# Optimization experiments

Hardware: AMD Instinct MI355X
Metric: run time of the kernel (lower is better)

Reference implementation:

```python
import jax, jax.numpy as jnp
import numpy as np

H = 16        # num_attention_heads
D = 1024      # hidden_size
HD = D // H   # attention_head_size = 64

def setup_inputs() -> dict:
    key = jax.random.key(0)
    ks = jax.random.split(key, 5)
    scale = 0.02
    return {
        "hidden_states": jax.random.normal(ks[0], (4, 2048, D), dtype=jnp.float32),
        "attention_mask": jnp.zeros((4, 2048), dtype=jnp.float32),
        "Wq": jax.random.normal(ks[1], (D, D), dtype=jnp.float32) * scale,
        "bq": jnp.zeros((D,), dtype=jnp.float32),
        "Wk": jax.random.normal(ks[2], (D, D), dtype=jnp.float32) * scale,
        "bk": jnp.zeros((D,), dtype=jnp.float32),
        "Wv": jax.random.normal(ks[3], (D, D), dtype=jnp.float32) * scale,
        "bv": jnp.zeros((D,), dtype=jnp.float32),
    }

def _heads(x, B, S):
    # [B,S,D] -> [B,H,S,HD]
    return x.reshape(B, S, H, HD).transpose(0, 2, 1, 3)

def reference(hidden_states, attention_mask, Wq, bq, Wk, bk, Wv, bv):
    B, S, _ = hidden_states.shape
    q = _heads(hidden_states @ Wq + bq, B, S)
    k = _heads(hidden_states @ Wk + bk, B, S)
    v = _heads(hidden_states @ Wv + bv, B, S)
    # scores: [B,H,S,S]
    scores = jnp.einsum('bhqd,bhkd->bhqk', q, k) / jnp.sqrt(jnp.float32(HD))
    scores = scores + attention_mask[:, None, None, :]  # additive mask
    probs = jax.nn.softmax(scores, axis=-1)
    # dropout is identity in eval mode
    ctx = jnp.einsum('bhqk,bhkd->bhqd', probs, v)
    return ctx.transpose(0, 2, 1, 3).reshape(B, S, H * HD)
```

## Files before the change

### kernel.cpp

```cpp
#include <hip/hip_runtime.h>


typedef __bf16 bf16_t;
typedef __bf16 bf16x2 __attribute__((ext_vector_type(2)));
typedef __bf16 bf16x4 __attribute__((ext_vector_type(4)));
typedef __bf16 bf16x8 __attribute__((ext_vector_type(8)));
typedef float floatx16 __attribute__((ext_vector_type(16)));
typedef float floatx4 __attribute__((ext_vector_type(4)));

__device__ __forceinline__ void glds16(const void* g, void* l) {
  __builtin_amdgcn_global_load_lds(
      (const __attribute__((address_space(1))) void*)g,
      (__attribute__((address_space(3))) void*)l, 16, 0, 0);
}

__device__ __forceinline__ float exp2_fast(float x) {
  return __builtin_amdgcn_exp2f(x);
}

__device__ __forceinline__ unsigned pk2(float a, float b) {
  union { bf16x2 v; unsigned u; } cv;
  cv.v[0] = (bf16_t)a; cv.v[1] = (bf16_t)b;
  return cv.u;
}

__global__ __launch_bounds__(256) void k_cvt_x(const float* __restrict__ X,
                                               bf16_t* __restrict__ Xb) {
  int i = (blockIdx.x * 256 + threadIdx.x) * 4;
  float4 v = *(const float4*)(X + i);
  bf16x4 o;
  o[0] = (bf16_t)v.x; o[1] = (bf16_t)v.y; o[2] = (bf16_t)v.z; o[3] = (bf16_t)v.w;
  *(bf16x4*)(Xb + i) = o;
}

__global__ __launch_bounds__(256) void k_tw(const float* __restrict__ Wq,
                                            const float* __restrict__ Wk,
                                            const float* __restrict__ Wv,
                                            bf16_t* __restrict__ Wt) {
  int z = blockIdx.z;
  const float* W = (z == 0) ? Wq : ((z == 1) ? Wk : Wv);
  bf16_t* dst = Wt + (size_t)z * 1048576;
  __shared__ float t[32][33];
  int tx = threadIdx.x & 31, ty = threadIdx.x >> 5;
  int bx = blockIdx.x, by = blockIdx.y;
#pragma unroll
  for (int r = 0; r < 4; r++) {
    int k = by * 32 + ty + r * 8;
    t[ty + r * 8][tx] = W[k * 1024 + bx * 32 + tx];
  }
  __syncthreads();
#pragma unroll
  for (int r = 0; r < 4; r++) {
    int n = bx * 32 + ty + r * 8;
    dst[(size_t)n * 1024 + by * 32 + tx] = (bf16_t)t[tx][ty + r * 8];
  }
}

__global__ __launch_bounds__(256) void k_qkv(
    const bf16_t* __restrict__ Xb, const bf16_t* __restrict__ Wt,
    const float* __restrict__ bq, const float* __restrict__ bk,
    const float* __restrict__ bv, bf16_t* __restrict__ Qb,
    bf16_t* __restrict__ Kb, bf16_t* __restrict__ Vt) {
  __shared__ bf16_t tA[128 * 64];
  __shared__ bf16_t tB[128 * 64];
  int tid = threadIdx.x, wv = tid >> 6, lane = tid & 63;
  int quad = lane >> 4, l16 = lane & 15;
  int wm = wv >> 1, wn = wv & 1;

  int id = blockIdx.x;
  int x = id & 7, w = id >> 3;
  int bn = w >> 3, pm = w & 7;
  int bm = x * 8 + pm;
  size_t m0 = (size_t)bm * 128, n0 = (size_t)bn * 128;
  int wsel = bn >> 3;

  floatx4 acc[4][4];
#pragma unroll
  for (int a = 0; a < 4; a++)
#pragma unroll
    for (int b = 0; b < 4; b++)
#pragma unroll
      for (int r = 0; r < 4; r++) acc[a][b][r] = 0.f;

  const bf16_t* Ab = Xb + m0 * 1024;
  const bf16_t* Bb = Wt + n0 * 1024;
  const bf16_t* fA = (wsel == 2) ? tB : tA;
  const bf16_t* fB = (wsel == 2) ? tA : tB;

  for (int k0 = 0; k0 < 1024; k0 += 64) {
    __syncthreads();
#pragma unroll
    for (int i = 0; i < 4; i++) {
      int j = wv * 4 + i;
      int row = j * 8 + (lane >> 3);
      int dblk = (lane & 7) ^ (row & 7);
      glds16(Ab + (size_t)row * 1024 + k0 + dblk * 8, tA + j * 512);
      glds16(Bb + (size_t)row * 1024 + k0 + dblk * 8, tB + j * 512);
    }
    __syncthreads();
#pragma unroll
    for (int s = 0; s < 2; s++) {
      bf16x8 av[4], bw[4];
#pragma unroll
      for (int rt = 0; rt < 4; rt++) {
        int rowa = wm * 64 + rt * 16 + l16;
        av[rt] = *(const bf16x8*)(fA + rowa * 64 + (((4 * s + quad) ^ (rowa & 7)) * 8));
        int rowb = wn * 64 + rt * 16 + l16;
        bw[rt] = *(const bf16x8*)(fB + rowb * 64 + (((4 * s + quad) ^ (rowb & 7)) * 8));
      }
#pragma unroll
      for (int rt = 0; rt < 4; rt++)
#pragma unroll
        for (int ct = 0; ct < 4; ct++)
          acc[rt][ct] = __builtin_amdgcn_mfma_f32_16x16x32_bf16(av[rt], bw[ct],
                                                               acc[rt][ct], 0, 0, 0);
    }
  }

  if (wsel == 2) {
    int bb = (int)(m0 >> 11);
#pragma unroll
    for (int rt = 0; rt < 4; rt++) {
#pragma unroll
      for (int r = 0; r < 4; r++) {
        int nl = wm * 64 + rt * 16 + quad * 4 + r;
        int n1 = ((int)n0 + nl) & 1023;
        int hh = n1 >> 6, dd = n1 & 63;
        float bi = bv[n1];
        size_t base = (size_t)(bb * 16 + hh) * 131072 + (size_t)dd * 2048;
#pragma unroll
        for (int ct = 0; ct < 4; ct++) {
          int m = (int)m0 + wn * 64 + ct * 16 + l16;
          Vt[base + (m & 2047)] = (bf16_t)(acc[rt][ct][r] + bi);
        }
      }
    }
  } else {
    const float* bias = (wsel == 0) ? bq : bk;
#pragma unroll
    for (int ct = 0; ct < 4; ct++) {
      int n = (int)n0 + wn * 64 + ct * 16 + l16;
      int n1 = n & 1023;
      int hh = n1 >> 6, dd = n1 & 63;
      float bi = bias[n1];
#pragma unroll
      for (int rt = 0; rt < 4; rt++) {
#pragma unroll
        for (int r = 0; r < 4; r++) {
          int m = (int)m0 + wm * 64 + rt * 16 + quad * 4 + r;
          int bb = m >> 11, ss = m & 2047;
          size_t bh = (size_t)(bb * 16 + hh);
          float v = acc[rt][ct][r] + bi;
          if (wsel == 0) {
            Qb[bh * 131072 + (size_t)ss * 64 + dd] = (bf16_t)(v * 0.18033688011117f);
          } else {
            Kb[bh * 131072 + (size_t)ss * 64 + dd] = (bf16_t)v;
          }
        }
      }
    }
  }
}

__global__ __launch_bounds__(256, 3) void k_attn(const bf16_t* __restrict__ Qb,
                                                 const bf16_t* __restrict__ Kb,
                                                 const bf16_t* __restrict__ VtG,
                                                 const float* __restrict__ mask,
                                                 float* __restrict__ out) {
  __shared__ float smem[10240];
  bf16_t* lds = (bf16_t*)smem;
  float* mlds = smem + 8192;

  int tid = threadIdx.x, wq = tid >> 6, lane = tid & 63;
  int q5 = lane & 31, h5 = lane >> 5;

  int id = blockIdx.x;
  int x = id & 7, w = id >> 3;
  int bh = x * 8 + (w >> 4), qt = w & 15;
  int b = bh >> 4, hh = bh & 15;

  const bf16_t* Qp = Qb + (size_t)bh * 131072;
  const bf16_t* Kp = Kb + (size_t)bh * 131072;
  const bf16_t* Vp = VtG + (size_t)bh * 131072;
  const float* mp = mask + b * 2048;

#pragma unroll
  for (int j = 0; j < 2; j++) {
    float4 mv = *(const float4*)(mp + tid * 8 + j * 4);
    float4 sv;
    sv.x = mv.x * 1.4426950408890f - 12.0f;
    sv.y = mv.y * 1.4426950408890f - 12.0f;
    sv.z = mv.z * 1.4426950408890f - 12.0f;
    sv.w = mv.w * 1.4426950408890f - 12.0f;
    *(float4*)(mlds + tid * 8 + j * 4) = sv;
  }

  int q0 = qt * 128 + wq * 32;
  bf16x8 qf[4];
#pragma unroll
  for (int s = 0; s < 4; s++)
    qf[s] = *(const bf16x8*)(Qp + (size_t)(q0 + q5) * 64 + s * 16 + h5 * 8);

  int off[2][4];
#pragma unroll
  for (int j = 0; j < 2; j++)
#pragma unroll
    for (int s = 0; s < 4; s++)
      off[j][s] = (j * 32 + q5) * 64 + (((2 * s + h5) ^ (q5 & 7)) * 8);

  int r0 = wq * 16 + (lane >> 3);
  int slot = (lane & 7) ^ ((lane >> 3) & 7);
  const bf16_t* kg0 = Kp + (size_t)r0 * 64 + slot * 8;
  const bf16_t* kg1 = kg0 + 512;
  const bf16_t* vg0 = Vp + (size_t)r0 * 2048 + slot * 8;
  const bf16_t* vg1 = vg0 + 16384;
  int c0 = wq * 2;

  floatx16 ov[2];
#pragma unroll
  for (int t2 = 0; t2 < 2; t2++)
#pragma unroll
    for (int r = 0; r < 16; r++) ov[t2][r] = 0.f;
  float p0 = 0.f, p1 = 0.f, p2 = 0.f, p3 = 0.f;

  {
    bf16_t* bK = lds;
    bf16_t* bV = lds + 4096;
    glds16(kg0, bK + c0 * 512); glds16(kg1, bK + c0 * 512 + 512);
    glds16(vg0, bV + c0 * 512); glds16(vg1, bV + c0 * 512 + 512);
    kg0 += 4096; kg1 += 4096; vg0 += 64; vg1 += 64;
  }

  for (int it = 0; it < 32; ++it) {
    int kk0 = it * 64, cur = it & 1;
    __syncthreads();
    if (it + 1 < 32) {
      bf16_t* bK = lds + (cur ^ 1) * 8192;
      bf16_t* bV = bK + 4096;
      glds16(kg0, bK + c0 * 512); glds16(kg1, bK + c0 * 512 + 512);
      glds16(vg0, bV + c0 * 512); glds16(vg1, bV + c0 * 512 + 512);
      kg0 += 4096; kg1 += 4096; vg0 += 64; vg1 += 64;
    }
    const bf16_t* bK = lds + cur * 8192;
    const bf16_t* bV = bK + 4096;

    floatx16 st[2];
#pragma unroll
    for (int tt = 0; tt < 2; tt++) {
      floatx16 a;
#pragma unroll
      for (int r = 0; r < 16; r++) a[r] = 0.f;
#pragma unroll
      for (int s = 0; s < 4; s++) {
        bf16x8 kf = *(const bf16x8*)(bK + off[tt][s]);
        a = __builtin_amdgcn_mfma_f32_32x32x16_bf16(kf, qf[s], a, 0, 0, 0);
      }
      st[tt] = a;
    }

#pragma unroll
    for (int tt = 0; tt < 2; tt++) {
#pragma unroll
      for (int g = 0; g < 4; g++) {
        float4 mv = *(const float4*)(mlds + kk0 + tt * 32 + g * 8 + h5 * 4);
        float e0 = exp2_fast(st[tt][g * 4 + 0] + mv.x);
        float e1 = exp2_fast(st[tt][g * 4 + 1] + mv.y);
        float e2 = exp2_fast(st[tt][g * 4 + 2] + mv.z);
        float e3 = exp2_fast(st[tt][g * 4 + 3] + mv.w);
        st[tt][g * 4 + 0] = e0; st[tt][g * 4 + 1] = e1;
        st[tt][g * 4 + 2] = e2; st[tt][g * 4 + 3] = e3;
        p0 += e0; p1 += e1; p2 += e2; p3 += e3;
      }
    }

#pragma unroll
    for (int s = 0; s < 4; s++) {
      int t = s >> 1, base = (s & 1) * 8;
      unsigned A  = pk2(st[t][base + 0], st[t][base + 1]);
      unsigned B2 = pk2(st[t][base + 2], st[t][base + 3]);
      unsigned C  = pk2(st[t][base + 4], st[t][base + 5]);
      unsigned D  = pk2(st[t][base + 6], st[t][base + 7]);
      unsigned s1 = h5 ? A : C, s2 = h5 ? B2 : D;
      unsigned r1 = (unsigned)__shfl_xor((int)s1, 32);
      unsigned r2 = (unsigned)__shfl_xor((int)s2, 32);
      union { uint4 u; bf16x8 v; } pf;
      pf.u.x = h5 ? r1 : A;  pf.u.y = h5 ? r2 : B2;
      pf.u.z = h5 ? C  : r1; pf.u.w = h5 ? D  : r2;
#pragma unroll
      for (int t2 = 0; t2 < 2; t2++) {
        bf16x8 vf = *(const bf16x8*)(bV + off[t2][s]);
        ov[t2] = __builtin_amdgcn_mfma_f32_32x32x16_bf16(vf, pf.v, ov[t2], 0, 0, 0);
      }
    }
  }

  float ls = (p0 + p1) + (p2 + p3);
  ls += __shfl_xor(ls, 32);
  float rl = 1.f / ls;

  __syncthreads();
#pragma unroll
  for (int t2 = 0; t2 < 2; t2++)
#pragma unroll
    for (int r = 0; r < 16; r++) {
      int d = t2 * 32 + (r & 3) + 8 * (r >> 2) + 4 * h5;
      smem[(wq * 32 + q5) * 68 + d] = ov[t2][r] * rl;
    }
  __syncthreads();
  int qbase = b * 2048 + qt * 128;
#pragma unroll
  for (int i = 0; i < 8; i++) {
    int slot2 = i * 256 + tid;
    int q = slot2 >> 4, c = slot2 & 15;
    float4 v = *(const float4*)(smem + q * 68 + c * 4);
    *(float4*)(out + (size_t)(qbase + q) * 1024 + hh * 64 + c * 4) = v;
  }
}

extern "C" void kernel_launch(void* const* d_in, const int* in_sizes, int n_in,
                              void* d_out, int out_size, void* d_ws, size_t ws_size,
                              hipStream_t stream) {
  const float* X    = (const float*)d_in[0];
  const float* mask = (const float*)d_in[1];
  const float* Wq   = (const float*)d_in[2];
  const float* bq   = (const float*)d_in[3];
  const float* Wk   = (const float*)d_in[4];
  const float* bk   = (const float*)d_in[5];
  const float* Wv   = (const float*)d_in[6];
  const float* bv   = (const float*)d_in[7];
  float* out = (float*)d_out;

  char* ws = (char*)d_ws;
  bf16_t* Xb = (bf16_t*)ws;
  bf16_t* Wt = (bf16_t*)(ws + 16777216);
  bf16_t* Qb = (bf16_t*)(ws + 23068672);
  bf16_t* Kb = (bf16_t*)(ws + 39845888);
  bf16_t* Vt = (bf16_t*)(ws + 56623104);

  k_cvt_x<<<8192, 256, 0, stream>>>(X, Xb);
  k_tw<<<dim3(32, 32, 3), 256, 0, stream>>>(Wq, Wk, Wv, Wt);
  k_qkv<<<1536, 256, 0, stream>>>(Xb, Wt, bq, bk, bv, Qb, Kb, Vt);
  k_attn<<<1024, 256, 0, stream>>>(Qb, Kb, Vt, mask, out);
}
```

Before: 253.1 us.

## Double attention block to 8 waves sharing each K/V tile

The attention kernel now launches 512 blocks of 512 threads, each covering 256 queries with 8 waves, so every K/V tile loaded into LDS feeds twice as many waves and each thread issues half as many global-to-LDS loads. The exp2 computation is also interleaved with the bf16 packing per sub-step, which should shorten register live ranges. The output epilogue is split into two halves that reuse the same LDS staging area. In exchange, barriers now synchronise 8 waves instead of 4, and the launch bounds change from 3 to 4 waves per EU, which may pressure registers.

```diff
diff --git a/kernel.cpp b/kernel.cpp
--- a/kernel.cpp
+++ b/kernel.cpp
@@ -162,12 +162,12 @@
   }
 }
 
-__global__ __launch_bounds__(256, 3) void k_attn(const bf16_t* __restrict__ Qb,
+__global__ __launch_bounds__(512, 4) void k_attn(const bf16_t* __restrict__ Qb,
                                                  const bf16_t* __restrict__ Kb,
                                                  const bf16_t* __restrict__ VtG,
                                                  const float* __restrict__ mask,
                                                  float* __restrict__ out) {
-  __shared__ float smem[10240];
+  __shared__ float smem[10752];
   bf16_t* lds = (bf16_t*)smem;
   float* mlds = smem + 8192;
 
@@ -176,7 +176,7 @@
 
   int id = blockIdx.x;
   int x = id & 7, w = id >> 3;
-  int bh = x * 8 + (w >> 4), qt = w & 15;
+  int bh = x * 8 + (w >> 3), qt8 = w & 7;
   int b = bh >> 4, hh = bh & 15;
 
   const bf16_t* Qp = Qb + (size_t)bh * 131072;
@@ -184,18 +184,17 @@
   const bf16_t* Vp = VtG + (size_t)bh * 131072;
   const float* mp = mask + b * 2048;
 
-#pragma unroll
-  for (int j = 0; j < 2; j++) {
-    float4 mv = *(const float4*)(mp + tid * 8 + j * 4);
+  {
+    float4 mv = *(const float4*)(mp + tid * 4);
     float4 sv;
     sv.x = mv.x * 1.4426950408890f - 12.0f;
     sv.y = mv.y * 1.4426950408890f - 12.0f;
     sv.z = mv.z * 1.4426950408890f - 12.0f;
     sv.w = mv.w * 1.4426950408890f - 12.0f;
-    *(float4*)(mlds + tid * 8 + j * 4) = sv;
-  }
-
-  int q0 = qt * 128 + wq * 32;
+    *(float4*)(mlds + tid * 4) = sv;
+  }
+
+  int q0 = qt8 * 256 + wq * 32;
   bf16x8 qf[4];
 #pragma unroll
   for (int s = 0; s < 4; s++)
@@ -208,13 +207,11 @@
     for (int s = 0; s < 4; s++)
       off[j][s] = (j * 32 + q5) * 64 + (((2 * s + h5) ^ (q5 & 7)) * 8);
 
-  int r0 = wq * 16 + (lane >> 3);
+  int r0 = wq * 8 + (lane >> 3);
   int slot = (lane & 7) ^ ((lane >> 3) & 7);
-  const bf16_t* kg0 = Kp + (size_t)r0 * 64 + slot * 8;
-  const bf16_t* kg1 = kg0 + 512;
-  const bf16_t* vg0 = Vp + (size_t)r0 * 2048 + slot * 8;
-  const bf16_t* vg1 = vg0 + 16384;
-  int c0 = wq * 2;
+  const bf16_t* kg = Kp + (size_t)r0 * 64 + slot * 8;
+  const bf16_t* vg = Vp + (size_t)r0 * 2048 + slot * 8;
+  int c512 = wq * 512;
 
   floatx16 ov[2];
 #pragma unroll
@@ -223,23 +220,18 @@
     for (int r = 0; r < 16; r++) ov[t2][r] = 0.f;
   float p0 = 0.f, p1 = 0.f, p2 = 0.f, p3 = 0.f;
 
-  {
-    bf16_t* bK = lds;
-    bf16_t* bV = lds + 4096;
-    glds16(kg0, bK + c0 * 512); glds16(kg1, bK + c0 * 512 + 512);
-    glds16(vg0, bV + c0 * 512); glds16(vg1, bV + c0 * 512 + 512);
-    kg0 += 4096; kg1 += 4096; vg0 += 64; vg1 += 64;
-  }
+  glds16(kg, lds + c512);
+  glds16(vg, lds + 4096 + c512);
+  kg += 4096; vg += 64;
 
   for (int it = 0; it < 32; ++it) {
     int kk0 = it * 64, cur = it & 1;
     __syncthreads();
     if (it + 1 < 32) {
-      bf16_t* bK = lds + (cur ^ 1) * 8192;
-      bf16_t* bV = bK + 4096;
-      glds16(kg0, bK + c0 * 512); glds16(kg1, bK + c0 * 512 + 512);
-      glds16(vg0, bV + c0 * 512); glds16(vg1, bV + c0 * 512 + 512);
-      kg0 += 4096; kg1 += 4096; vg0 += 64; vg1 += 64;
+      bf16_t* bKn = lds + (cur ^ 1) * 8192;
+      glds16(kg, bKn + c512);
+      glds16(vg, bKn + 4096 + c512);
+      kg += 4096; vg += 64;
     }
     const bf16_t* bK = lds + cur * 8192;
     const bf16_t* bV = bK + 4096;
@@ -259,27 +251,24 @@
     }
 
 #pragma unroll
-    for (int tt = 0; tt < 2; tt++) {
-#pragma unroll
-      for (int g = 0; g < 4; g++) {
-        float4 mv = *(const float4*)(mlds + kk0 + tt * 32 + g * 8 + h5 * 4);
-        float e0 = exp2_fast(st[tt][g * 4 + 0] + mv.x);
-        float e1 = exp2_fast(st[tt][g * 4 + 1] + mv.y);
-        float e2 = exp2_fast(st[tt][g * 4 + 2] + mv.z);
-        float e3 = exp2_fast(st[tt][g * 4 + 3] + mv.w);
-        st[tt][g * 4 + 0] = e0; st[tt][g * 4 + 1] = e1;
-        st[tt][g * 4 + 2] = e2; st[tt][g * 4 + 3] = e3;
-        p0 += e0; p1 += e1; p2 += e2; p3 += e3;
-      }
-    }
-
-#pragma unroll
     for (int s = 0; s < 4; s++) {
       int t = s >> 1, base = (s & 1) * 8;
-      unsigned A  = pk2(st[t][base + 0], st[t][base + 1]);
-      unsigned B2 = pk2(st[t][base + 2], st[t][base + 3]);
-      unsigned C  = pk2(st[t][base + 4], st[t][base + 5]);
-      unsigned D  = pk2(st[t][base + 6], st[t][base + 7]);
+      int g0 = (s & 1) * 2;
+      float4 m0v = *(const float4*)(mlds + kk0 + t * 32 + g0 * 8 + h5 * 4);
+      float4 m1v = *(const float4*)(mlds + kk0 + t * 32 + (g0 + 1) * 8 + h5 * 4);
+      float e0 = exp2_fast(st[t][base + 0] + m0v.x);
+      float e1 = exp2_fast(st[t][base + 1] + m0v.y);
+      float e2 = exp2_fast(st[t][base + 2] + m0v.z);
+      float e3 = exp2_fast(st[t][base + 3] + m0v.w);
+      float e4 = exp2_fast(st[t][base + 4] + m1v.x);
+      float e5 = exp2_fast(st[t][base + 5] + m1v.y);
+      float e6 = exp2_fast(st[t][base + 6] + m1v.z);
+      float e7 = exp2_fast(st[t][base + 7] + m1v.w);
+      p0 += e0 + e4; p1 += e1 + e5; p2 += e2 + e6; p3 += e3 + e7;
+      unsigned A  = pk2(e0, e1);
+      unsigned B2 = pk2(e2, e3);
+      unsigned C  = pk2(e4, e5);
+      unsigned D  = pk2(e6, e7);
       unsigned s1 = h5 ? A : C, s2 = h5 ? B2 : D;
       unsigned r1 = (unsigned)__shfl_xor((int)s1, 32);
       unsigned r2 = (unsigned)__shfl_xor((int)s2, 32);
@@ -298,22 +287,29 @@
   ls += __shfl_xor(ls, 32);
   float rl = 1.f / ls;
 
-  __syncthreads();
-#pragma unroll
-  for (int t2 = 0; t2 < 2; t2++)
-#pragma unroll
-    for (int r = 0; r < 16; r++) {
-      int d = t2 * 32 + (r & 3) + 8 * (r >> 2) + 4 * h5;
-      smem[(wq * 32 + q5) * 68 + d] = ov[t2][r] * rl;
-    }
-  __syncthreads();
-  int qbase = b * 2048 + qt * 128;
-#pragma unroll
-  for (int i = 0; i < 8; i++) {
-    int slot2 = i * 256 + tid;
-    int q = slot2 >> 4, c = slot2 & 15;
-    float4 v = *(const float4*)(smem + q * 68 + c * 4);
-    *(float4*)(out + (size_t)(qbase + q) * 1024 + hh * 64 + c * 4) = v;
+  int qbase0 = b * 2048 + qt8 * 256;
+#pragma unroll
+  for (int half = 0; half < 2; half++) {
+    __syncthreads();
+    if ((wq >> 2) == half) {
+      int qloc = (wq & 3) * 32 + q5;
+#pragma unroll
+      for (int t2 = 0; t2 < 2; t2++)
+#pragma unroll
+        for (int r = 0; r < 16; r++) {
+          int d = t2 * 32 + (r & 3) + 8 * (r >> 2) + 4 * h5;
+          smem[qloc * 68 + d] = ov[t2][r] * rl;
+        }
+    }
+    __syncthreads();
+    int qbase = qbase0 + half * 128;
+#pragma unroll
+    for (int i = 0; i < 4; i++) {
+      int slot2 = i * 512 + tid;
+      int q = slot2 >> 4, c = slot2 & 15;
+      float4 v = *(const float4*)(smem + q * 68 + c * 4);
+      *(float4*)(out + (size_t)(qbase + q) * 1024 + hh * 64 + c * 4) = v;
+    }
   }
 }
 
@@ -340,5 +336,5 @@
   k_cvt_x<<<8192, 256, 0, stream>>>(X, Xb);
   k_tw<<<dim3(32, 32, 3), 256, 0, stream>>>(Wq, Wk, Wv, Wt);
   k_qkv<<<1536, 256, 0, stream>>>(Xb, Wt, bq, bk, bv, Qb, Kb, Vt);
-  k_attn<<<1024, 256, 0, stream>>>(Qb, Kb, Vt, mask, out);
-}
+  k_attn<<<512, 512, 0, stream>>>(Qb, Kb, Vt, mask, out);
+}
```

After: 246.2 us. 1.03x faster.

## Double query rows per attention wave, fold mask into MFMA, merge prep kernels

Applied to the files above, without the earlier changes.

Each attention wave now handles 64 query rows instead of 32, so every K/V tile loaded into LDS feeds twice as many MFMAs and the grid halves to 512 blocks. The additive mask is applied through an extra MFMA with a one-hot Q fragment instead of per-element VALU adds, and the epilogue writes output in two halves through shared memory. The X conversion and weight transpose kernels are merged into one launch. The cost is higher register pressure (occupancy hint lowered from 3 to 2), fewer blocks in flight, and the mask value being rounded to bf16.

```diff
diff --git a/kernel.cpp b/kernel.cpp
--- a/kernel.cpp
+++ b/kernel.cpp
@@ -24,35 +24,38 @@
   return cv.u;
 }
 
-__global__ __launch_bounds__(256) void k_cvt_x(const float* __restrict__ X,
-                                               bf16_t* __restrict__ Xb) {
-  int i = (blockIdx.x * 256 + threadIdx.x) * 4;
-  float4 v = *(const float4*)(X + i);
-  bf16x4 o;
-  o[0] = (bf16_t)v.x; o[1] = (bf16_t)v.y; o[2] = (bf16_t)v.z; o[3] = (bf16_t)v.w;
-  *(bf16x4*)(Xb + i) = o;
-}
-
-__global__ __launch_bounds__(256) void k_tw(const float* __restrict__ Wq,
-                                            const float* __restrict__ Wk,
-                                            const float* __restrict__ Wv,
-                                            bf16_t* __restrict__ Wt) {
-  int z = blockIdx.z;
-  const float* W = (z == 0) ? Wq : ((z == 1) ? Wk : Wv);
-  bf16_t* dst = Wt + (size_t)z * 1048576;
-  __shared__ float t[32][33];
-  int tx = threadIdx.x & 31, ty = threadIdx.x >> 5;
-  int bx = blockIdx.x, by = blockIdx.y;
-#pragma unroll
-  for (int r = 0; r < 4; r++) {
-    int k = by * 32 + ty + r * 8;
-    t[ty + r * 8][tx] = W[k * 1024 + bx * 32 + tx];
-  }
-  __syncthreads();
-#pragma unroll
-  for (int r = 0; r < 4; r++) {
-    int n = bx * 32 + ty + r * 8;
-    dst[(size_t)n * 1024 + by * 32 + tx] = (bf16_t)t[tx][ty + r * 8];
+__global__ __launch_bounds__(256) void k_prep(const float* __restrict__ X,
+                                              bf16_t* __restrict__ Xb,
+                                              const float* __restrict__ Wq,
+                                              const float* __restrict__ Wk,
+                                              const float* __restrict__ Wv,
+                                              bf16_t* __restrict__ Wt) {
+  int bid = blockIdx.x;
+  if (bid < 8192) {
+    int i = (bid * 256 + threadIdx.x) * 4;
+    float4 v = *(const float4*)(X + i);
+    bf16x4 o;
+    o[0] = (bf16_t)v.x; o[1] = (bf16_t)v.y; o[2] = (bf16_t)v.z; o[3] = (bf16_t)v.w;
+    *(bf16x4*)(Xb + i) = o;
+  } else {
+    int t = bid - 8192;
+    int z = t >> 10, r2 = t & 1023;
+    int bx = r2 & 31, by = r2 >> 5;
+    const float* W = (z == 0) ? Wq : ((z == 1) ? Wk : Wv);
+    bf16_t* dst = Wt + (size_t)z * 1048576;
+    __shared__ float tt[32][33];
+    int tx = threadIdx.x & 31, ty = threadIdx.x >> 5;
+#pragma unroll
+    for (int r = 0; r < 4; r++) {
+      int k = by * 32 + ty + r * 8;
+      tt[ty + r * 8][tx] = W[k * 1024 + bx * 32 + tx];
+    }
+    __syncthreads();
+#pragma unroll
+    for (int r = 0; r < 4; r++) {
+      int n = bx * 32 + ty + r * 8;
+      dst[(size_t)n * 1024 + by * 32 + tx] = (bf16_t)tt[tx][ty + r * 8];
+    }
   }
 }
 
@@ -162,7 +165,7 @@
   }
 }
 
-__global__ __launch_bounds__(256, 3) void k_attn(const bf16_t* __restrict__ Qb,
+__global__ __launch_bounds__(256, 2) void k_attn(const bf16_t* __restrict__ Qb,
                                                  const bf16_t* __restrict__ Kb,
                                                  const bf16_t* __restrict__ VtG,
                                                  const float* __restrict__ mask,
@@ -176,7 +179,7 @@
 
   int id = blockIdx.x;
   int x = id & 7, w = id >> 3;
-  int bh = x * 8 + (w >> 4), qt = w & 15;
+  int bh = x * 8 + (w >> 3), qt = w & 7;
   int b = bh >> 4, hh = bh & 15;
 
   const bf16_t* Qp = Qb + (size_t)bh * 131072;
@@ -195,11 +198,17 @@
     *(float4*)(mlds + tid * 8 + j * 4) = sv;
   }
 
-  int q0 = qt * 128 + wq * 32;
-  bf16x8 qf[4];
-#pragma unroll
-  for (int s = 0; s < 4; s++)
-    qf[s] = *(const bf16x8*)(Qp + (size_t)(q0 + q5) * 64 + s * 16 + h5 * 8);
+  int q0 = qt * 256 + wq * 64;
+  bf16x8 qf0[4], qf1[4];
+#pragma unroll
+  for (int s = 0; s < 4; s++) {
+    qf0[s] = *(const bf16x8*)(Qp + (size_t)(q0 + q5) * 64 + s * 16 + h5 * 8);
+    qf1[s] = *(const bf16x8*)(Qp + (size_t)(q0 + 32 + q5) * 64 + s * 16 + h5 * 8);
+  }
+
+  union { uint4 u; bf16x8 v; } qfe;
+  qfe.u.x = h5 ? 0u : 0x00003f80u;
+  qfe.u.y = 0u; qfe.u.z = 0u; qfe.u.w = 0u;
 
   int off[2][4];
 #pragma unroll
@@ -216,12 +225,13 @@
   const bf16_t* vg1 = vg0 + 16384;
   int c0 = wq * 2;
 
-  floatx16 ov[2];
-#pragma unroll
-  for (int t2 = 0; t2 < 2; t2++)
+  floatx16 ov[4];
+#pragma unroll
+  for (int t2 = 0; t2 < 4; t2++)
 #pragma unroll
     for (int r = 0; r < 16; r++) ov[t2][r] = 0.f;
-  float p0 = 0.f, p1 = 0.f, p2 = 0.f, p3 = 0.f;
+  float pa0 = 0.f, pa1 = 0.f, pa2 = 0.f, pa3 = 0.f;
+  float pb0 = 0.f, pb1 = 0.f, pb2 = 0.f, pb3 = 0.f;
 
   {
     bf16_t* bK = lds;
@@ -244,76 +254,107 @@
     const bf16_t* bK = lds + cur * 8192;
     const bf16_t* bV = bK + 4096;
 
-    floatx16 st[2];
 #pragma unroll
     for (int tt = 0; tt < 2; tt++) {
-      floatx16 a;
-#pragma unroll
-      for (int r = 0; r < 16; r++) a[r] = 0.f;
+      floatx16 a0, a1;
+#pragma unroll
+      for (int r = 0; r < 16; r++) { a0[r] = 0.f; a1[r] = 0.f; }
 #pragma unroll
       for (int s = 0; s < 4; s++) {
         bf16x8 kf = *(const bf16x8*)(bK + off[tt][s]);
-        a = __builtin_amdgcn_mfma_f32_32x32x16_bf16(kf, qf[s], a, 0, 0, 0);
-      }
-      st[tt] = a;
-    }
-
-#pragma unroll
-    for (int tt = 0; tt < 2; tt++) {
-#pragma unroll
-      for (int g = 0; g < 4; g++) {
-        float4 mv = *(const float4*)(mlds + kk0 + tt * 32 + g * 8 + h5 * 4);
-        float e0 = exp2_fast(st[tt][g * 4 + 0] + mv.x);
-        float e1 = exp2_fast(st[tt][g * 4 + 1] + mv.y);
-        float e2 = exp2_fast(st[tt][g * 4 + 2] + mv.z);
-        float e3 = exp2_fast(st[tt][g * 4 + 3] + mv.w);
-        st[tt][g * 4 + 0] = e0; st[tt][g * 4 + 1] = e1;
-        st[tt][g * 4 + 2] = e2; st[tt][g * 4 + 3] = e3;
-        p0 += e0; p1 += e1; p2 += e2; p3 += e3;
-      }
-    }
-
-#pragma unroll
-    for (int s = 0; s < 4; s++) {
-      int t = s >> 1, base = (s & 1) * 8;
-      unsigned A  = pk2(st[t][base + 0], st[t][base + 1]);
-      unsigned B2 = pk2(st[t][base + 2], st[t][base + 3]);
-      unsigned C  = pk2(st[t][base + 4], st[t][base + 5]);
-      unsigned D  = pk2(st[t][base + 6], st[t][base + 7]);
-      unsigned s1 = h5 ? A : C, s2 = h5 ? B2 : D;
-      unsigned r1 = (unsigned)__shfl_xor((int)s1, 32);
-      unsigned r2 = (unsigned)__shfl_xor((int)s2, 32);
-      union { uint4 u; bf16x8 v; } pf;
-      pf.u.x = h5 ? r1 : A;  pf.u.y = h5 ? r2 : B2;
-      pf.u.z = h5 ? C  : r1; pf.u.w = h5 ? D  : r2;
-#pragma unroll
-      for (int t2 = 0; t2 < 2; t2++) {
-        bf16x8 vf = *(const bf16x8*)(bV + off[t2][s]);
-        ov[t2] = __builtin_amdgcn_mfma_f32_32x32x16_bf16(vf, pf.v, ov[t2], 0, 0, 0);
-      }
-    }
-  }
-
-  float ls = (p0 + p1) + (p2 + p3);
-  ls += __shfl_xor(ls, 32);
-  float rl = 1.f / ls;
-
-  __syncthreads();
-#pragma unroll
-  for (int t2 = 0; t2 < 2; t2++)
-#pragma unroll
-    for (int r = 0; r < 16; r++) {
-      int d = t2 * 32 + (r & 3) + 8 * (r >> 2) + 4 * h5;
-      smem[(wq * 32 + q5) * 68 + d] = ov[t2][r] * rl;
-    }
-  __syncthreads();
-  int qbase = b * 2048 + qt * 128;
-#pragma unroll
-  for (int i = 0; i < 8; i++) {
-    int slot2 = i * 256 + tid;
-    int q = slot2 >> 4, c = slot2 & 15;
-    float4 v = *(const float4*)(smem + q * 68 + c * 4);
-    *(float4*)(out + (size_t)(qbase + q) * 1024 + hh * 64 + c * 4) = v;
+        a0 = __builtin_amdgcn_mfma_f32_32x32x16_bf16(kf, qf0[s], a0, 0, 0, 0);
+        a1 = __builtin_amdgcn_mfma_f32_32x32x16_bf16(kf, qf1[s], a1, 0, 0, 0);
+      }
+      {
+        float ml = mlds[kk0 + tt * 32 + q5];
+        union { uint4 u; bf16x8 v; } kfe;
+        kfe.u.x = h5 ? 0u : pk2(ml, 0.f);
+        kfe.u.y = 0u; kfe.u.z = 0u; kfe.u.w = 0u;
+        a0 = __builtin_amdgcn_mfma_f32_32x32x16_bf16(kfe.v, qfe.v, a0, 0, 0, 0);
+        a1 = __builtin_amdgcn_mfma_f32_32x32x16_bf16(kfe.v, qfe.v, a1, 0, 0, 0);
+      }
+
+#pragma unroll
+      for (int sl = 0; sl < 2; sl++) {
+        int s = tt * 2 + sl, base = sl * 8;
+        float e0 = exp2_fast(a0[base + 0]);
+        float e1 = exp2_fast(a0[base + 1]);
+        float e2 = exp2_fast(a0[base + 2]);
+        float e3 = exp2_fast(a0[base + 3]);
+        float e4 = exp2_fast(a0[base + 4]);
+        float e5 = exp2_fast(a0[base + 5]);
+        float e6 = exp2_fast(a0[base + 6]);
+        float e7 = exp2_fast(a0[base + 7]);
+        pa0 += e0 + e4; pa1 += e1 + e5; pa2 += e2 + e6; pa3 += e3 + e7;
+        unsigned A0 = pk2(e0, e1), B0 = pk2(e2, e3);
+        unsigned C0 = pk2(e4, e5), D0 = pk2(e6, e7);
+        float f0 = exp2_fast(a1[base + 0]);
+        float f1 = exp2_fast(a1[base + 1]);
+        float f2 = exp2_fast(a1[base + 2]);
+        float f3 = exp2_fast(a1[base + 3]);
+        float f4 = exp2_fast(a1[base + 4]);
+        float f5 = exp2_fast(a1[base + 5]);
+        float f6 = exp2_fast(a1[base + 6]);
+        float f7 = exp2_fast(a1[base + 7]);
+        pb0 += f0 + f4; pb1 += f1 + f5; pb2 += f2 + f6; pb3 += f3 + f7;
+        unsigned A1 = pk2(f0, f1), B1 = pk2(f2, f3);
+        unsigned C1 = pk2(f4, f5), D1 = pk2(f6, f7);
+        unsigned s10 = h5 ? A0 : C0, s20 = h5 ? B0 : D0;
+        unsigned s11 = h5 ? A1 : C1, s21 = h5 ? B1 : D1;
+        unsigned r10 = (unsigned)__shfl_xor((int)s10, 32);
+        unsigned r20 = (unsigned)__shfl_xor((int)s20, 32);
+        unsigned r11 = (unsigned)__shfl_xor((int)s11, 32);
+        unsigned r21 = (unsigned)__shfl_xor((int)s21, 32);
+        union { uint4 u; bf16x8 v; } pf0, pf1;
+        pf0.u.x = h5 ? r10 : A0;  pf0.u.y = h5 ? r20 : B0;
+        pf0.u.z = h5 ? C0  : r10; pf0.u.w = h5 ? D0  : r20;
+        pf1.u.x = h5 ? r11 : A1;  pf1.u.y = h5 ? r21 : B1;
+        pf1.u.z = h5 ? C1  : r11; pf1.u.w = h5 ? D1  : r21;
+#pragma unroll
+        for (int t2 = 0; t2 < 2; t2++) {
+          bf16x8 vf = *(const bf16x8*)(bV + off[t2][s]);
+          ov[t2]     = __builtin_amdgcn_mfma_f32_32x32x16_bf16(vf, pf0.v, ov[t2], 0, 0, 0);
+          ov[2 + t2] = __builtin_amdgcn_mfma_f32_32x32x16_bf16(vf, pf1.v, ov[2 + t2], 0, 0, 0);
+        }
+      }
+    }
+  }
+
+  float ls0 = (pa0 + pa1) + (pa2 + pa3);
+  float ls1 = (pb0 + pb1) + (pb2 + pb3);
+  ls0 += __shfl_xor(ls0, 32);
+  ls1 += __shfl_xor(ls1, 32);
+  float rl0 = 1.f / ls0, rl1 = 1.f / ls1;
+
+  int qbase0 = b * 2048 + qt * 256;
+#pragma unroll
+  for (int half = 0; half < 2; half++) {
+    __syncthreads();
+    if ((wq >> 1) == half) {
+      int qloc = (wq & 1) * 128;
+      int qw = (wq & 1) * 64;
+#pragma unroll
+      for (int u = 0; u < 2; u++) {
+        float rl = u ? rl1 : rl0;
+#pragma unroll
+        for (int t2 = 0; t2 < 2; t2++)
+#pragma unroll
+          for (int r = 0; r < 16; r++) {
+            int d = t2 * 32 + (r & 3) + 8 * (r >> 2) + 4 * h5;
+            smem[(qw + u * 32 + q5) * 68 + d] = ov[u * 2 + t2][r] * rl;
+          }
+      }
+      (void)qloc;
+    }
+    __syncthreads();
+    int qbase = qbase0 + half * 128;
+#pragma unroll
+    for (int i = 0; i < 8; i++) {
+      int slot2 = i * 256 + tid;
+      int q = slot2 >> 4, c = slot2 & 15;
+      float4 v = *(const float4*)(smem + q * 68 + c * 4);
+      *(float4*)(out + (size_t)(qbase + q) * 1024 + hh * 64 + c * 4) = v;
+    }
   }
 }
 
@@ -337,8 +378,7 @@
   bf16_t* Kb = (bf16_t*)(ws + 39845888);
   bf16_t* Vt = (bf16_t*)(ws + 56623104);
 
-  k_cvt_x<<<8192, 256, 0, stream>>>(X, Xb);
-  k_tw<<<dim3(32, 32, 3), 256, 0, stream>>>(Wq, Wk, Wv, Wt);
+  k_prep<<<11264, 256, 0, stream>>>(X, Xb, Wq, Wk, Wv, Wt);
   k_qkv<<<1536, 256, 0, stream>>>(Xb, Wt, bq, bk, bv, Qb, Kb, Vt);
-  k_attn<<<1024, 256, 0, stream>>>(Qb, Kb, Vt, mask, out);
-}
+  k_attn<<<512, 256, 0, stream>>>(Qb, Kb, Vt, mask, out);
+}
```

Result: faster. 239.8 us (-5.2%).
